# Optimization experiments

Measured on AMD Instinct MI355X. Metric: run time of the kernel, lower is better.

Reference implementation:

```python
import jax, jax.numpy as jnp
import numpy as np

B, N, C, K, S = 4, 4096, 256, 16, 1  # batch, points, channels, knn, share_planes
A = C // S  # attn_planes
EPS = 1e-5


def setup_inputs() -> dict:
    key = jax.random.key(0)
    ks = jax.random.split(key, 16)
    rn = lambda k, shape, s=0.05: (jax.random.normal(k, shape, jnp.float32) * s)
    return {
        "xyz": jax.random.uniform(ks[0], (B, N, 3), jnp.float32),
        "features": jax.random.normal(ks[1], (B, N, C), jnp.float32),
        "wq": rn(ks[2], (C, C)), "bq": jnp.zeros((C,), jnp.float32),
        "wk": rn(ks[3], (C, C)), "bk": jnp.zeros((C,), jnp.float32),
        "wv": rn(ks[4], (C, C)), "bv": jnp.zeros((C,), jnp.float32),
        "d1_w": rn(ks[5], (3, 3), 0.3), "d1_b": jnp.zeros((3,), jnp.float32),
        "bn_d_g": jnp.ones((3,), jnp.float32), "bn_d_b": jnp.zeros((3,), jnp.float32),
        "d2_w": rn(ks[6], (3, C), 0.3), "d2_b": jnp.zeros((C,), jnp.float32),
        "g_bn1_g": jnp.ones((C,), jnp.float32), "g_bn1_b": jnp.zeros((C,), jnp.float32),
        "g1_w": rn(ks[7], (C, A)), "g1_b": jnp.zeros((A,), jnp.float32),
        "g_bn2_g": jnp.ones((A,), jnp.float32), "g_bn2_b": jnp.zeros((A,), jnp.float32),
        "g2_w": rn(ks[8], (A, A)), "g2_b": jnp.zeros((A,), jnp.float32),
    }


def _bn(x, g, b):
    # BatchNorm2d_P in training mode: channels-last tensor (B,N,K,Ch),
    # normalize over all dims except the channel axis (biased variance).
    m = jnp.mean(x, axis=(0, 1, 2))
    v = jnp.var(x, axis=(0, 1, 2))
    return (x - m) * jax.lax.rsqrt(v + EPS) * g + b


def reference(xyz, features, wq, bq, wk, bk, wv, bv,
              d1_w, d1_b, bn_d_g, bn_d_b, d2_w, d2_b,
              g_bn1_g, g_bn1_b, g1_w, g1_b, g_bn2_g, g_bn2_b, g2_w, g2_b):
    # --- KNN (square_distance + topk smallest) ---
    sq = jnp.sum(xyz * xyz, axis=-1)                                  # (B,N)
    dist = sq[:, :, None] + sq[:, None, :] - 2.0 * jnp.einsum('bnd,bmd->bnm', xyz, xyz)
    idx = jax.lax.top_k(-dist, K)[1]                                  # (B,N,K)

    gather = jax.vmap(lambda pts, i: pts[i])                          # index_points
    knn_xyz = gather(xyz, idx)                                        # (B,N,K,3)

    q = features @ wq + bq                                            # (B,N,C)
    k = gather(features @ wk + bk, idx)                               # (B,N,K,C)
    v = gather(features @ wv + bv, idx)                               # (B,N,K,C)

    # fc_delta: Linear(3,3) -> BN -> ReLU -> Linear(3,C)
    rel = xyz[:, :, None, :] - knn_xyz                                # (B,N,K,3)
    pos_enc = jax.nn.relu(_bn(rel @ d1_w + d1_b, bn_d_g, bn_d_b)) @ d2_w + d2_b  # (B,N,K,C)

    # grouped sum of pos_enc over share_planes (identity when S=1)
    pe_sum = pos_enc.reshape(B, N, K, S, C // S).sum(axis=3)          # (B,N,K,C/S)

    # fc_gamma: BN -> ReLU -> Linear(C,A) -> BN -> ReLU -> Linear(A,A)
    h = q[:, :, None, :] - k + pe_sum                                 # (B,N,K,C)
    h = jax.nn.relu(_bn(h, g_bn1_g, g_bn1_b)) @ g1_w + g1_b           # (B,N,K,A)
    attn = jax.nn.relu(_bn(h, g_bn2_g, g_bn2_b)) @ g2_w + g2_b        # (B,N,K,A)
    attn = jax.nn.softmax(attn, axis=-2)                              # softmax over K

    vg = (v + pos_enc).reshape(B, N, K, S, C // S)                    # (B,N,K,S,C/S)
    out = jnp.einsum('bnksa,bnka->bnsa', vg, attn)                    # (B,N,S,C/S)
    return out.reshape(B, N, C)
```

## Files before the change

### kernel.cpp

```cpp
#include <hip/hip_runtime.h>
#include <hip/hip_bf16.h>
#include <math.h>

#define BB 4
#define NN 4096
#define CC 256
#define KK 16
#define AA 256
#define NPTS (BB*NN)
#define BNKTOT (NPTS*KK)
#define EPSF 1e-5f
#define MINVF (1.0f/262144.0f)

#define WPB 4
#define MROWS (WPB*KK)
#define IMG_PER_KSTEP (256*40)
#define IMG_TOTAL (8*IMG_PER_KSTEP)

#define ST_BND_SUM 0
#define ST_BND_SQ  8
#define ST_G1_SUM  16
#define ST_G1_SQ   272
#define ST_G2_SUM  528
#define ST_G2_SQ   784
#define CO_BND_S   0
#define CO_BND_B   4
#define CO_G1_S    16
#define CO_G1_B    272
#define CO_G2_S    528
#define CO_G2_B    784

typedef unsigned short u16;
typedef __attribute__((ext_vector_type(8))) short bf16x8;
typedef __attribute__((ext_vector_type(4))) float f32x4;

__device__ inline u16 f2bf(float x) {
    unsigned u = __float_as_uint(x);
    unsigned r = (u + 0x7FFFu + ((u >> 16) & 1u)) >> 16;
    return (u16)r;
}

__device__ inline float waveReduceAdd(float v) {
    #pragma unroll
    for (int o = 32; o > 0; o >>= 1) v += __shfl_down(v, o);
    return v;
}

__device__ inline bool lexlt(float d1, int i1, float d2, int i2) {
    return (d1 < d2) || (d1 == d2 && i1 < i2);
}

__global__ __launch_bounds__(256, 2) void qkv_mfma(
    const float* __restrict__ feat, const u16* __restrict__ wimg_all,
    const float* __restrict__ bq, const float* __restrict__ bk, const float* __restrict__ bv,
    float* __restrict__ oq, float* __restrict__ ok, float* __restrict__ ov)
{
    const int t = threadIdx.x;
    const int l = t & 63, w = t >> 6;
    const int p0 = blockIdx.x * 64;
    const u16* img = wimg_all + (size_t)blockIdx.y * IMG_TOTAL;
    const float* bias = blockIdx.y == 0 ? bq : (blockIdx.y == 1 ? bk : bv);
    float* out = blockIdx.y == 0 ? oq : (blockIdx.y == 1 ? ok : ov);

    __shared__ __align__(16) u16 A_lds[64 * 256];
    __shared__ __align__(16) u16 B_lds[IMG_PER_KSTEP];

    for (int r = 0; r < 64; ++r)
        A_lds[(r * 256 + t) ^ ((r & 7) << 3)] = f2bf(feat[(size_t)(p0 + r) * CC + t]);
    __syncthreads();

    f32x4 acc[4][4];
    #pragma unroll
    for (int q = 0; q < 4; ++q) {
        const float gb = bias[(w*4 + q) * 16 + (l & 15)];
        #pragma unroll
        for (int m = 0; m < 4; ++m) acc[m][q] = (f32x4){gb, gb, gb, gb};
    }

    for (int s = 0; s < 8; ++s) {
        #pragma unroll
        for (int i = 0; i < 5; ++i) {
            const int e = t + i * 256;
            *(uint4*)&B_lds[e * 8] = *(const uint4*)&img[(size_t)s * IMG_PER_KSTEP + e * 8];
        }
        __syncthreads();
        bf16x8 bf[4];
        #pragma unroll
        for (int q = 0; q < 4; ++q)
            bf[q] = *(const bf16x8*)&B_lds[((w*4 + q) * 16 + (l & 15)) * 40 + (l >> 4) * 8];
        #pragma unroll
        for (int m = 0; m < 4; ++m) {
            const int r = m * 16 + (l & 15);
            const bf16x8 af = *(const bf16x8*)&A_lds[((r * 256 + s * 32 + (l >> 4) * 8)) ^ ((r & 7) << 3)];
            #pragma unroll
            for (int q = 0; q < 4; ++q)
                acc[m][q] = __builtin_amdgcn_mfma_f32_16x16x32_bf16(af, bf[q], acc[m][q], 0, 0, 0);
        }
        __syncthreads();
    }

    #pragma unroll
    for (int q = 0; q < 4; ++q) {
        const int a = (w*4 + q) * 16 + (l & 15);
        #pragma unroll
        for (int m = 0; m < 4; ++m)
            #pragma unroll
            for (int j = 0; j < 4; ++j)
                out[(size_t)(p0 + m*16 + (l >> 4)*4 + j) * CC + a] = acc[m][q][j];
    }
}

__global__ __launch_bounds__(256, 2) void qkv_kernel(
    const float* __restrict__ feat,
    const float* __restrict__ wq, const float* __restrict__ bq,
    const float* __restrict__ wk, const float* __restrict__ bk,
    const float* __restrict__ wv, const float* __restrict__ bv,
    float* __restrict__ oq, float* __restrict__ ok, float* __restrict__ ov)
{
    const float* W; const float* bias; float* out;
    if (blockIdx.y == 0)      { W = wq; bias = bq; out = oq; }
    else if (blockIdx.y == 1) { W = wk; bias = bk; out = ok; }
    else                      { W = wv; bias = bv; out = ov; }

    const int p0 = blockIdx.x * 64;
    const int t  = threadIdx.x;
    __shared__ __align__(16) float fs[64][65];

    float acc[64];
    #pragma unroll
    for (int p = 0; p < 64; ++p) acc[p] = 0.f;

    for (int it = 0; it < 4; ++it) {
        const int tp = t >> 2;
        #pragma unroll
        for (int q = 0; q < 4; ++q) {
            const int ch = (t & 3) + q * 4;
            float4 v = *(const float4*)&feat[(size_t)(p0 + tp) * CC + it * 64 + ch * 4];
            fs[tp][ch*4+0] = v.x; fs[tp][ch*4+1] = v.y; fs[tp][ch*4+2] = v.z; fs[tp][ch*4+3] = v.w;
        }
        __syncthreads();
        #pragma unroll 4
        for (int i = 0; i < 64; ++i) {
            const float w = W[(size_t)(it * 64 + i) * CC + t];
            #pragma unroll
            for (int p = 0; p < 64; ++p) acc[p] = fmaf(fs[p][i], w, acc[p]);
        }
        __syncthreads();
    }
    const float bv_ = bias[t];
    #pragma unroll
    for (int p = 0; p < 64; ++p) out[(size_t)(p0 + p) * CC + t] = acc[p] + bv_;
}

#define KNN_BUFCAP 48
__global__ __launch_bounds__(256) void knn_kernel(
    const float* __restrict__ xyz, int* __restrict__ idxout)
{
    const int t = threadIdx.x;
    const int l = t & 63;
    const int w = t >> 6;
    const int g = blockIdx.x * 4 + w;
    const int b = g >> 12;
    const int n = g & 4095;
    const float* xb = xyz + (size_t)b * NN * 3;

    const float qx = xb[n*3+0], qy = xb[n*3+1], qz = xb[n*3+2];
    const float sqn = qx*qx + qy*qy + qz*qz;

    __shared__ float4 tile[512];
    __shared__ float bufd[4][KNN_BUFCAP];
    __shared__ int   bufi[4][KNN_BUFCAP];

    const float INF = 3.0e38f;
    float ld = INF; int li = 0x7fffffff;
    float kd = INF; int ki = 0x7fffffff;
    int cnt = 0;

    for (int t0 = 0; t0 < NN; t0 += 512) {
        #pragma unroll
        for (int r = 0; r < 2; ++r) {
            const int j = t + r * 256;
            const float x = xb[(t0 + j)*3 + 0];
            const float y = xb[(t0 + j)*3 + 1];
            const float z = xb[(t0 + j)*3 + 2];
            tile[j] = make_float4(x, y, z, x*x + y*y + z*z);
        }
        __syncthreads();
        for (int j0 = 0; j0 < 512; j0 += 64) {
            const float4 p = tile[j0 + l];
            const float d = sqn + p.w - 2.0f * (qx*p.x + qy*p.y + qz*p.z);
            const int  ci = t0 + j0 + l;
            bool pass = lexlt(d, ci, kd, ki);
            while (__any(pass)) {
                const unsigned long long m = __ballot(pass);
                const int rank  = (int)__popcll(m & ((1ull << l) - 1ull));
                const int total = (int)__popcll(m);
                const int space = KNN_BUFCAP - cnt;
                if (pass && rank < space) {
                    bufd[w][cnt + rank] = d;
                    bufi[w][cnt + rank] = ci;
                    pass = false;
                }
                cnt += total < space ? total : space;
                if (__any(pass)) {
                    float sd; int si;
                    if (l < 16)            { sd = ld; si = li; }
                    else if (l - 16 < cnt) { sd = bufd[w][l-16]; si = bufi[w][l-16]; }
                    else                   { sd = INF; si = 0x7fffffff; }
                    #pragma unroll
                    for (int k = 2; k <= 64; k <<= 1) {
                        #pragma unroll
                        for (int jj = k >> 1; jj > 0; jj >>= 1) {
                            const float od = __shfl_xor(sd, jj);
                            const int   oi = __shfl_xor(si, jj);
                            const bool keepMin = (((l & jj) == 0) == ((l & k) == 0));
                            const bool oSm = lexlt(od, oi, sd, si);
                            if (keepMin ? oSm : !oSm) { sd = od; si = oi; }
                        }
                    }
                    ld = (l < 16) ? sd : INF;
                    li = (l < 16) ? si : 0x7fffffff;
                    kd = __shfl(sd, 15);
                    ki = __shfl(si, 15);
                    cnt = 0;
                    pass = pass && lexlt(d, ci, kd, ki);
                }
            }
        }
        __syncthreads();
    }

    if (cnt > 0) {
        float sd; int si;
        if (l < 16)            { sd = ld; si = li; }
        else if (l - 16 < cnt) { sd = bufd[w][l-16]; si = bufi[w][l-16]; }
        else                   { sd = INF; si = 0x7fffffff; }
        #pragma unroll
        for (int k = 2; k <= 64; k <<= 1) {
            #pragma unroll
            for (int jj = k >> 1; jj > 0; jj >>= 1) {
                const float od = __shfl_xor(sd, jj);
                const int   oi = __shfl_xor(si, jj);
                const bool keepMin = (((l & jj) == 0) == ((l & k) == 0));
                const bool oSm = lexlt(od, oi, sd, si);
                if (keepMin ? oSm : !oSm) { sd = od; si = oi; }
            }
        }
        li = si;
    }
    if (l < 16) idxout[((size_t)b * NN + n) * KK + l] = li;
}

__global__ __launch_bounds__(256) void fc_delta_kernel(
    const float* __restrict__ xyz, const int* __restrict__ idx,
    const float* __restrict__ d1w, const float* __restrict__ d1b,
    float* __restrict__ t3, float* __restrict__ stats)
{
    const int t = threadIdx.x;
    float s[3] = {0.f, 0.f, 0.f}, sq[3] = {0.f, 0.f, 0.f};

    #pragma unroll
    for (int it = 0; it < 4; ++it) {
        const int g = blockIdx.x * 1024 + it * 256 + t;
        const int b = g >> 16;
        const int n = (g & 65535) >> 4;
        const int mi = idx[g];
        const float* xb = xyz + (size_t)b * NN * 3;
        const float rx = xb[n*3+0] - xb[mi*3+0];
        const float ry = xb[n*3+1] - xb[mi*3+1];
        const float rz = xb[n*3+2] - xb[mi*3+2];
        #pragma unroll
        for (int j = 0; j < 3; ++j) {
            const float tv = fmaf(rx, d1w[0*3+j], fmaf(ry, d1w[1*3+j], fmaf(rz, d1w[2*3+j], d1b[j])));
            t3[(size_t)g*3 + j] = tv;
            s[j] += tv;
            sq[j] = fmaf(tv, tv, sq[j]);
        }
    }

    __shared__ float red[4][6];
    const int lane = t & 63, wv = t >> 6;
    #pragma unroll
    for (int j = 0; j < 3; ++j) {
        const float rs  = waveReduceAdd(s[j]);
        const float rsq = waveReduceAdd(sq[j]);
        if (lane == 0) { red[wv][j] = rs; red[wv][3+j] = rsq; }
    }
    __syncthreads();
    if (t < 6) {
        const float v = red[0][t] + red[1][t] + red[2][t] + red[3][t];
        atomicAdd(&stats[t < 3 ? ST_BND_SUM + t : ST_BND_SQ + (t-3)], v);
    }
}

__global__ void finalize_bnd(const float* __restrict__ stats,
                             const float* __restrict__ g, const float* __restrict__ b,
                             float* __restrict__ consts)
{
    const int t = threadIdx.x;
    if (t < 3) {
        const float m = stats[ST_BND_SUM + t] * MINVF;
        const float v = stats[ST_BND_SQ + t] * MINVF - m * m;
        const float s = g[t] / sqrtf(v + EPSF);
        consts[CO_BND_S + t] = s;
        consts[CO_BND_B + t] = b[t] - m * s;
    }
}

__global__ __launch_bounds__(256, 2) void bn1_stats_kernel(
    const float* __restrict__ qproj, const float* __restrict__ kproj,
    const float* __restrict__ t3, const int* __restrict__ idx,
    const float* __restrict__ consts,
    const float* __restrict__ d2w, const float* __restrict__ d2b,
    float* __restrict__ stats)
{
    const int b   = blockIdx.x >> 8;
    const int pt0 = (blockIdx.x & 255) * 16;
    const int t = threadIdx.x;

    __shared__ float a3[768];
    __shared__ int idxs[256];

    const float bs[3]  = {consts[CO_BND_S+0], consts[CO_BND_S+1], consts[CO_BND_S+2]};
    const float bsh[3] = {consts[CO_BND_B+0], consts[CO_BND_B+1], consts[CO_BND_B+2]};
    const float* t3b = t3 + (size_t)(b * NN + pt0) * KK * 3;
    #pragma unroll
    for (int q = 0; q < 3; ++q) {
        const int f = t + q * 256;
        const int j = f % 3;
        a3[f] = fmaxf(fmaf(t3b[f], bs[j], bsh[j]), 0.f);
    }
    idxs[t] = idx[(size_t)(b * NN + pt0) * KK + t];
    __syncthreads();

    const int c = t;
    const float d20 = d2w[c], d21 = d2w[CC + c], d22 = d2w[2*CC + c], d2bc = d2b[c];
    float s = 0.f, sq = 0.f;
    for (int p = 0; p < 16; ++p) {
        const float qv = qproj[(size_t)(b * NN + pt0 + p) * CC + c];
        #pragma unroll
        for (int k = 0; k < 16; ++k) {
            const int mi = idxs[p*16 + k];
            const float kv = kproj[((size_t)b * NN + mi) * CC + c];
            const int f = (p*16 + k) * 3;
            const float pe = fmaf(a3[f], d20, fmaf(a3[f+1], d21, fmaf(a3[f+2], d22, d2bc)));
            const float h = qv - kv + pe;
            s += h; sq = fmaf(h, h, sq);
        }
    }
    atomicAdd(&stats[ST_G1_SUM + c], s);
    atomicAdd(&stats[ST_G1_SQ + c], sq);
}

__global__ void finalize_g(const float* __restrict__ ssum, const float* __restrict__ ssq,
                           const float* __restrict__ g, const float* __restrict__ b,
                           float* __restrict__ os, float* __restrict__ ob)
{
    const int c = threadIdx.x;
    const float m = ssum[c] * MINVF;
    const float v = ssq[c] * MINVF - m * m;
    const float s = g[c] / sqrtf(v + EPSF);
    os[c] = s;
    ob[c] = b[c] - m * s;
}

__global__ __launch_bounds__(256) void prep_weights(
    const float* __restrict__ wq, const float* __restrict__ wk,
    const float* __restrict__ wv, const float* __restrict__ g1w,
    const float* __restrict__ g2w, u16* __restrict__ img_all)
{
    const int s = blockIdx.x;
    const int mat = blockIdx.y;
    const float* W = mat == 0 ? wq : mat == 1 ? wk : mat == 2 ? wv : mat == 3 ? g1w : g2w;
    u16* img = img_all + (size_t)mat * IMG_TOTAL + (size_t)s * IMG_PER_KSTEP;
    const int n = threadIdx.x;
    #pragma unroll
    for (int i = 0; i < 32; ++i) {
        img[n*40 + i] = f2bf(W[(size_t)(s*32 + i) * AA + n]);
    }
}

__global__ __launch_bounds__(256, 2) void stage3_mfma(
    const float* __restrict__ qproj, const float* __restrict__ kproj,
    const float* __restrict__ t3, const int* __restrict__ idx,
    const float* __restrict__ consts, float* __restrict__ stats,
    const float* __restrict__ d2w, const float* __restrict__ d2b,
    const u16* __restrict__ g1img, const float* __restrict__ g1b,
    __hip_bfloat16* __restrict__ h2)
{
    const int t = threadIdx.x;
    const int l = t & 63, w = t >> 6;
    const int pt0 = blockIdx.x * WPB;
    const int bI = pt0 >> 12;

    __shared__ __align__(16) u16 A_lds[MROWS * 256];
    __shared__ __align__(16) u16 B_lds[IMG_PER_KSTEP];
    __shared__ int   idxs[MROWS];
    __shared__ float a3s[MROWS * 3];

    if (t < MROWS) idxs[t] = idx[(size_t)pt0 * KK + t];
    if (t < MROWS * 3) {
        const int j = t % 3;
        a3s[t] = fmaxf(fmaf(t3[(size_t)pt0 * 48 + t], consts[CO_BND_S + j], consts[CO_BND_B + j]), 0.f);
    }
    __syncthreads();

    {
        const float d20 = d2w[t], d21 = d2w[CC + t], d22 = d2w[2*CC + t], d2bc = d2b[t];
        const float g1s = consts[CO_G1_S + t], g1sh = consts[CO_G1_B + t];
        float qv[WPB];
        #pragma unroll
        for (int p = 0; p < WPB; ++p) qv[p] = qproj[(size_t)(pt0 + p) * CC + t];
        for (int r = 0; r < MROWS; ++r) {
            const int mi = idxs[r];
            const float kv = kproj[((size_t)bI * NN + mi) * CC + t];
            const float pe = fmaf(a3s[r*3], d20, fmaf(a3s[r*3+1], d21, fmaf(a3s[r*3+2], d22, d2bc)));
            const float h = qv[r >> 4] - kv + pe;
            const float av = fmaxf(fmaf(h, g1s, g1sh), 0.f);
            A_lds[(r * 256 + t) ^ ((r & 7) << 3)] = f2bf(av);
        }
    }
    __syncthreads();

    f32x4 acc[4][4];
    #pragma unroll
    for (int q = 0; q < 4; ++q) {
        const float gb = g1b[(w*4 + q) * 16 + (l & 15)];
        #pragma unroll
        for (int m = 0; m < 4; ++m) acc[m][q] = (f32x4){gb, gb, gb, gb};
    }

    for (int s = 0; s < 8; ++s) {
        #pragma unroll
        for (int i = 0; i < 5; ++i) {
            const int e = t + i * 256;
            *(uint4*)&B_lds[e * 8] = *(const uint4*)&g1img[(size_t)s * IMG_PER_KSTEP + e * 8];
        }
        __syncthreads();
        bf16x8 bf[4];
        #pragma unroll
        for (int q = 0; q < 4; ++q)
            bf[q] = *(const bf16x8*)&B_lds[((w*4 + q) * 16 + (l & 15)) * 40 + (l >> 4) * 8];
        #pragma unroll
        for (int m = 0; m < 4; ++m) {
            const int r = m * 16 + (l & 15);
            const bf16x8 af = *(const bf16x8*)&A_lds[((r * 256 + s * 32 + (l >> 4) * 8)) ^ ((r & 7) << 3)];
            #pragma unroll
            for (int q = 0; q < 4; ++q)
                acc[m][q] = __builtin_amdgcn_mfma_f32_16x16x32_bf16(af, bf[q], acc[m][q], 0, 0, 0);
        }
        __syncthreads();
    }

    #pragma unroll
    for (int q = 0; q < 4; ++q) {
        const int a = (w*4 + q) * 16 + (l & 15);
        float sc = 0.f, sq = 0.f;
        #pragma unroll
        for (int m = 0; m < 4; ++m) {
            #pragma unroll
            for (int j = 0; j < 4; ++j) {
                const float v = acc[m][q][j];
                sc += v; sq = fmaf(v, v, sq);
                h2[((size_t)(pt0 + m) * KK + ((l >> 4) * 4 + j)) * AA + a] = __float2bfloat16(v);
            }
        }
        sc += __shfl_xor(sc, 16); sc += __shfl_xor(sc, 32);
        sq += __shfl_xor(sq, 16); sq += __shfl_xor(sq, 32);
        if (l < 16) {
            atomicAdd(&stats[ST_G2_SUM + a], sc);
            atomicAdd(&stats[ST_G2_SQ + a], sq);
        }
    }
}

__global__ __launch_bounds__(256, 2) void stage4_mfma(
    const float* __restrict__ vproj,
    const float* __restrict__ t3, const int* __restrict__ idx,
    const float* __restrict__ consts,
    const float* __restrict__ d2w, const float* __restrict__ d2b,
    const u16* __restrict__ g2img, const float* __restrict__ g2b,
    const __hip_bfloat16* __restrict__ h2, float* __restrict__ out)
{
    const int t = threadIdx.x;
    const int l = t & 63, w = t >> 6;
    const int pt0 = blockIdx.x * WPB;
    const int bI = pt0 >> 12;

    __shared__ __align__(16) u16 A_lds[MROWS * 256];
    __shared__ __align__(16) u16 B_lds[IMG_PER_KSTEP];
    __shared__ int   idxs[MROWS];
    __shared__ float a3s[MROWS * 3];

    if (t < MROWS) idxs[t] = idx[(size_t)pt0 * KK + t];
    if (t < MROWS * 3) {
        const int j = t % 3;
        a3s[t] = fmaxf(fmaf(t3[(size_t)pt0 * 48 + t], consts[CO_BND_S + j], consts[CO_BND_B + j]), 0.f);
    }
    __syncthreads();

    {
        const float g2s = consts[CO_G2_S + t], g2sh = consts[CO_G2_B + t];
        for (int r = 0; r < MROWS; ++r) {
            const float hv = __bfloat162float(h2[((size_t)pt0 * KK + r) * AA + t]);
            const float av = fmaxf(fmaf(hv, g2s, g2sh), 0.f);
            A_lds[(r * 256 + t) ^ ((r & 7) << 3)] = f2bf(av);
        }
    }
    __syncthreads();

    f32x4 acc[4][4];
    #pragma unroll
    for (int q = 0; q < 4; ++q) {
        const float gb = g2b[(w*4 + q) * 16 + (l & 15)];
        #pragma unroll
        for (int m = 0; m < 4; ++m) acc[m][q] = (f32x4){gb, gb, gb, gb};
    }

    for (int s = 0; s < 8; ++s) {
        #pragma unroll
        for (int i = 0; i < 5; ++i) {
            const int e = t + i * 256;
            *(uint4*)&B_lds[e * 8] = *(const uint4*)&g2img[(size_t)s * IMG_PER_KSTEP + e * 8];
        }
        __syncthreads();
        bf16x8 bf[4];
        #pragma unroll
        for (int q = 0; q < 4; ++q)
            bf[q] = *(const bf16x8*)&B_lds[((w*4 + q) * 16 + (l & 15)) * 40 + (l >> 4) * 8];
        #pragma unroll
        for (int m = 0; m < 4; ++m) {
            const int r = m * 16 + (l & 15);
            const bf16x8 af = *(const bf16x8*)&A_lds[((r * 256 + s * 32 + (l >> 4) * 8)) ^ ((r & 7) << 3)];
            #pragma unroll
            for (int q = 0; q < 4; ++q)
                acc[m][q] = __builtin_amdgcn_mfma_f32_16x16x32_bf16(af, bf[q], acc[m][q], 0, 0, 0);
        }
        __syncthreads();
    }

    #pragma unroll
    for (int q = 0; q < 4; ++q) {
        const int a = (w*4 + q) * 16 + (l & 15);
        const float dw0 = d2w[a], dw1 = d2w[CC + a], dw2 = d2w[2*CC + a], db = d2b[a];
        #pragma unroll
        for (int m = 0; m < 4; ++m) {
            f32x4 lg = acc[m][q];
            float mx = fmaxf(fmaxf(lg[0], lg[1]), fmaxf(lg[2], lg[3]));
            mx = fmaxf(mx, __shfl_xor(mx, 16));
            mx = fmaxf(mx, __shfl_xor(mx, 32));
            float e[4]; float ss = 0.f;
            #pragma unroll
            for (int j = 0; j < 4; ++j) { e[j] = expf(lg[j] - mx); ss += e[j]; }
            ss += __shfl_xor(ss, 16); ss += __shfl_xor(ss, 32);
            const float inv = 1.0f / ss;
            float part = 0.f;
            #pragma unroll
            for (int j = 0; j < 4; ++j) {
                const int kk = (l >> 4) * 4 + j;
                const int mi = idxs[m * 16 + kk];
                const float vv = vproj[((size_t)bI * NN + mi) * CC + a];
                const float pe = fmaf(a3s[(m*16+kk)*3], dw0,
                                 fmaf(a3s[(m*16+kk)*3+1], dw1,
                                 fmaf(a3s[(m*16+kk)*3+2], dw2, db)));
                part = fmaf(e[j] * inv, vv + pe, part);
            }
            part += __shfl_xor(part, 16); part += __shfl_xor(part, 32);
            if (l < 16) out[(size_t)(pt0 + m) * CC + a] = part;
        }
    }
}

__global__ __launch_bounds__(256, 2) void stage3_fp32(
    const float* __restrict__ qproj, const float* __restrict__ kproj,
    const float* __restrict__ t3, const int* __restrict__ idx,
    const float* __restrict__ consts, float* __restrict__ stats,
    const float* __restrict__ d2w, const float* __restrict__ d2b,
    const float* __restrict__ g1w, const float* __restrict__ g1b)
{
    const size_t pt = blockIdx.x;
    const int b = (int)(pt >> 12);
    const int t = threadIdx.x;
    __shared__ float a3[48];
    __shared__ int idxs[16];
    __shared__ __align__(16) float hr[16][256];
    if (t < 48) {
        const int j = t % 3;
        a3[t] = fmaxf(fmaf(t3[pt*48 + t], consts[CO_BND_S + j], consts[CO_BND_B + j]), 0.f);
    }
    if (t < 16) idxs[t] = idx[pt*16 + t];
    __syncthreads();
    {
        const float d20 = d2w[t], d21 = d2w[CC + t], d22 = d2w[2*CC + t], d2bc = d2b[t];
        const float g1s = consts[CO_G1_S + t], g1sh = consts[CO_G1_B + t];
        const float qv = qproj[pt * CC + t];
        #pragma unroll
        for (int k = 0; k < 16; ++k) {
            const int mi = idxs[k];
            const float kv = kproj[((size_t)b * NN + mi) * CC + t];
            const float pe = fmaf(a3[k*3], d20, fmaf(a3[k*3+1], d21, fmaf(a3[k*3+2], d22, d2bc)));
            hr[k][t] = fmaxf(fmaf(qv - kv + pe, g1s, g1sh), 0.f);
        }
    }
    __syncthreads();
    float acc[16];
    const float gb = g1b[t];
    #pragma unroll
    for (int k = 0; k < 16; ++k) acc[k] = gb;
    #pragma unroll 4
    for (int c4 = 0; c4 < 64; ++c4) {
        const float* wp = g1w + (size_t)(c4*4) * AA + t;
        const float w0 = wp[0], w1 = wp[AA], w2 = wp[2*AA], w3 = wp[3*AA];
        #pragma unroll
        for (int k = 0; k < 16; ++k) {
            const float4 hv = *(const float4*)&hr[k][c4*4];
            acc[k] = fmaf(hv.x, w0, fmaf(hv.y, w1, fmaf(hv.z, w2, fmaf(hv.w, w3, acc[k]))));
        }
    }
    float s = 0.f, sq = 0.f;
    #pragma unroll
    for (int k = 0; k < 16; ++k) { s += acc[k]; sq = fmaf(acc[k], acc[k], sq); }
    atomicAdd(&stats[ST_G2_SUM + t], s);
    atomicAdd(&stats[ST_G2_SQ + t], sq);
}

__global__ __launch_bounds__(256, 2) void stage4_fp32(
    const float* __restrict__ qproj, const float* __restrict__ kproj,
    const float* __restrict__ vproj,
    const float* __restrict__ t3, const int* __restrict__ idx,
    const float* __restrict__ consts,
    const float* __restrict__ d2w, const float* __restrict__ d2b,
    const float* __restrict__ g1w, const float* __restrict__ g1b,
    const float* __restrict__ g2w, const float* __restrict__ g2b,
    float* __restrict__ out)
{
    const size_t pt = blockIdx.x;
    const int b = (int)(pt >> 12);
    const int t = threadIdx.x;
    __shared__ float a3[48];
    __shared__ int idxs[16];
    __shared__ __align__(16) float r2[16][256];
    if (t < 48) {
        const int j = t % 3;
        a3[t] = fmaxf(fmaf(t3[pt*48 + t], consts[CO_BND_S + j], consts[CO_BND_B + j]), 0.f);
    }
    if (t < 16) idxs[t] = idx[pt*16 + t];
    __syncthreads();
    const float g2s = consts[CO_G2_S + t], g2sh = consts[CO_G2_B + t];
    {
        __shared__ __align__(16) float hr[16][256];
        {
            const float d20 = d2w[t], d21 = d2w[CC + t], d22 = d2w[2*CC + t], d2bc = d2b[t];
            const float g1s = consts[CO_G1_S + t], g1sh = consts[CO_G1_B + t];
            const float qv = qproj[pt * CC + t];
            #pragma unroll
            for (int k = 0; k < 16; ++k) {
                const int mi = idxs[k];
                const float kv = kproj[((size_t)b * NN + mi) * CC + t];
                const float pe = fmaf(a3[k*3], d20, fmaf(a3[k*3+1], d21, fmaf(a3[k*3+2], d22, d2bc)));
                hr[k][t] = fmaxf(fmaf(qv - kv + pe, g1s, g1sh), 0.f);
            }
        }
        __syncthreads();
        float acc[16];
        const float gb = g1b[t];
        #pragma unroll
        for (int k = 0; k < 16; ++k) acc[k] = gb;
        #pragma unroll 4
        for (int c4 = 0; c4 < 64; ++c4) {
            const float* wp = g1w + (size_t)(c4*4) * AA + t;
            const float w0 = wp[0], w1 = wp[AA], w2 = wp[2*AA], w3 = wp[3*AA];
            #pragma unroll
            for (int k = 0; k < 16; ++k) {
                const float4 hv = *(const float4*)&hr[k][c4*4];
                acc[k] = fmaf(hv.x, w0, fmaf(hv.y, w1, fmaf(hv.z, w2, fmaf(hv.w, w3, acc[k]))));
            }
        }
        __syncthreads();
        #pragma unroll
        for (int k = 0; k < 16; ++k) r2[k][t] = fmaxf(fmaf(acc[k], g2s, g2sh), 0.f);
        __syncthreads();
    }
    float lg[16];
    const float gb2 = g2b[t];
    #pragma unroll
    for (int k = 0; k < 16; ++k) lg[k] = gb2;
    #pragma unroll 4
    for (int c4 = 0; c4 < 64; ++c4) {
        const float* wp = g2w + (size_t)(c4*4) * AA + t;
        const float w0 = wp[0], w1 = wp[AA], w2 = wp[2*AA], w3 = wp[3*AA];
        #pragma unroll
        for (int k = 0; k < 16; ++k) {
            const float4 hv = *(const float4*)&r2[k][c4*4];
            lg[k] = fmaf(hv.x, w0, fmaf(hv.y, w1, fmaf(hv.z, w2, fmaf(hv.w, w3, lg[k]))));
        }
    }
    float mx = lg[0];
    #pragma unroll
    for (int k = 1; k < 16; ++k) mx = fmaxf(mx, lg[k]);
    float sum = 0.f;
    #pragma unroll
    for (int k = 0; k < 16; ++k) { lg[k] = expf(lg[k] - mx); sum += lg[k]; }
    const float inv = 1.0f / sum;
    const float d20 = d2w[t], d21 = d2w[CC + t], d22 = d2w[2*CC + t], d2bc = d2b[t];
    float o = 0.f;
    #pragma unroll
    for (int k = 0; k < 16; ++k) {
        const int mi = idxs[k];
        const float vv = vproj[((size_t)b * NN + mi) * CC + t];
        const float pe = fmaf(a3[k*3], d20, fmaf(a3[k*3+1], d21, fmaf(a3[k*3+2], d22, d2bc)));
        o = fmaf(vv + pe, lg[k] * inv, o);
    }
    out[pt * CC + t] = o;
}

extern "C" void kernel_launch(void* const* d_in, const int* in_sizes, int n_in,
                              void* d_out, int out_size, void* d_ws, size_t ws_size,
                              hipStream_t stream)
{
    const float* xyz   = (const float*)d_in[0];
    const float* feat  = (const float*)d_in[1];
    const float* wq    = (const float*)d_in[2];
    const float* bq    = (const float*)d_in[3];
    const float* wk    = (const float*)d_in[4];
    const float* bk    = (const float*)d_in[5];
    const float* wv    = (const float*)d_in[6];
    const float* bv    = (const float*)d_in[7];
    const float* d1w   = (const float*)d_in[8];
    const float* d1b   = (const float*)d_in[9];
    const float* bndg  = (const float*)d_in[10];
    const float* bndb  = (const float*)d_in[11];
    const float* d2w   = (const float*)d_in[12];
    const float* d2b   = (const float*)d_in[13];
    const float* g1g   = (const float*)d_in[14];
    const float* g1bb  = (const float*)d_in[15];
    const float* g1w   = (const float*)d_in[16];
    const float* g1b   = (const float*)d_in[17];
    const float* g2g   = (const float*)d_in[18];
    const float* g2bb  = (const float*)d_in[19];
    const float* g2w   = (const float*)d_in[20];
    const float* g2b   = (const float*)d_in[21];
    float* out = (float*)d_out;

    float* qproj = (float*)d_ws;
    float* kproj = qproj + (size_t)NPTS * CC;
    float* vproj = kproj + (size_t)NPTS * CC;
    float* t3    = vproj + (size_t)NPTS * CC;
    float* stats = t3 + (size_t)BNKTOT * 3;
    float* consts = stats + 2048;
    int*   idxb  = (int*)(consts + 2048);
    u16*   wimg  = (u16*)(idxb + BNKTOT);
    u16*   g1img = wimg + (size_t)3 * IMG_TOTAL;
    u16*   g2img = wimg + (size_t)4 * IMG_TOTAL;
    __hip_bfloat16* h2 = (__hip_bfloat16*)(wimg + (size_t)5 * IMG_TOTAL);
    const size_t need_store = (size_t)((char*)h2 - (char*)d_ws) + (size_t)BNKTOT * AA * 2;
    const bool store = ws_size >= need_store;

    hipMemsetAsync(stats, 0, 2048 * sizeof(float), stream);

    if (store) {
        prep_weights<<<dim3(8, 5), 256, 0, stream>>>(wq, wk, wv, g1w, g2w, wimg);
        qkv_mfma<<<dim3(NPTS / 64, 3), 256, 0, stream>>>(feat, wimg, bq, bk, bv,
                                                         qproj, kproj, vproj);
    } else {
        dim3 gq(NPTS / 64, 3);
        qkv_kernel<<<gq, 256, 0, stream>>>(feat, wq, bq, wk, bk, wv, bv, qproj, kproj, vproj);
    }

    knn_kernel<<<NPTS / 4, 256, 0, stream>>>(xyz, idxb);

    fc_delta_kernel<<<BNKTOT / 1024, 256, 0, stream>>>(xyz, idxb, d1w, d1b, t3, stats);

    finalize_bnd<<<1, 64, 0, stream>>>(stats, bndg, bndb, consts);

    bn1_stats_kernel<<<1024, 256, 0, stream>>>(qproj, kproj, t3, idxb, consts, d2w, d2b, stats);

    finalize_g<<<1, 256, 0, stream>>>(stats + ST_G1_SUM, stats + ST_G1_SQ, g1g, g1bb,
                                      consts + CO_G1_S, consts + CO_G1_B);

    if (store)
        stage3_mfma<<<NPTS / WPB, 256, 0, stream>>>(qproj, kproj, t3, idxb, consts, stats,
                                                    d2w, d2b, g1img, g1b, h2);
    else
        stage3_fp32<<<NPTS, 256, 0, stream>>>(qproj, kproj, t3, idxb, consts, stats,
                                              d2w, d2b, g1w, g1b);

    finalize_g<<<1, 256, 0, stream>>>(stats + ST_G2_SUM, stats + ST_G2_SQ, g2g, g2bb,
                                      consts + CO_G2_S, consts + CO_G2_B);

    if (store)
        stage4_mfma<<<NPTS / WPB, 256, 0, stream>>>(vproj, t3, idxb, consts,
                                                    d2w, d2b, g2img, g2b, h2, out);
    else
        stage4_fp32<<<NPTS, 256, 0, stream>>>(qproj, kproj, vproj, t3, idxb, consts,
                                              d2w, d2b, g1w, g1b, g2w, g2b, out);
}
```

Baseline: 681.9 us.

## Load MFMA weight fragments directly from global memory instead of LDS staging

The three MFMA GEMM kernels now read their bf16x8 B fragments straight from a repacked global weight image instead of copying each k-step slice into shared memory. prep_weights emits the image in fragment order, and the padded 40-element stride goes away. This removes two barriers per k-step and roughly 20 KB of LDS per block, which may raise occupancy. In exchange, each wave issues its own global/L2 loads for weights, and different waves no longer share a single copy.

```diff
diff --git a/kernel.cpp b/kernel.cpp
--- a/kernel.cpp
+++ b/kernel.cpp
@@ -14,7 +14,7 @@
 
 #define WPB 4
 #define MROWS (WPB*KK)
-#define IMG_PER_KSTEP (256*40)
+#define IMG_PER_KSTEP (256*32)
 #define IMG_TOTAL (8*IMG_PER_KSTEP)
 
 #define ST_BND_SUM 0
@@ -63,7 +63,6 @@
     float* out = blockIdx.y == 0 ? oq : (blockIdx.y == 1 ? ok : ov);
 
     __shared__ __align__(16) u16 A_lds[64 * 256];
-    __shared__ __align__(16) u16 B_lds[IMG_PER_KSTEP];
 
     for (int r = 0; r < 64; ++r)
         A_lds[(r * 256 + t) ^ ((r & 7) << 3)] = f2bf(feat[(size_t)(p0 + r) * CC + t]);
@@ -78,16 +77,12 @@
     }
 
     for (int s = 0; s < 8; ++s) {
-        #pragma unroll
-        for (int i = 0; i < 5; ++i) {
-            const int e = t + i * 256;
-            *(uint4*)&B_lds[e * 8] = *(const uint4*)&img[(size_t)s * IMG_PER_KSTEP + e * 8];
-        }
-        __syncthreads();
         bf16x8 bf[4];
         #pragma unroll
-        for (int q = 0; q < 4; ++q)
-            bf[q] = *(const bf16x8*)&B_lds[((w*4 + q) * 16 + (l & 15)) * 40 + (l >> 4) * 8];
+        for (int q = 0; q < 4; ++q) {
+            const int nq = (w*4 + q) * 16 + (l & 15);
+            bf[q] = *(const bf16x8*)&img[(size_t)s * IMG_PER_KSTEP + ((nq*4 + (l >> 4)) * 8)];
+        }
         #pragma unroll
         for (int m = 0; m < 4; ++m) {
             const int r = m * 16 + (l & 15);
@@ -96,7 +91,6 @@
             for (int q = 0; q < 4; ++q)
                 acc[m][q] = __builtin_amdgcn_mfma_f32_16x16x32_bf16(af, bf[q], acc[m][q], 0, 0, 0);
         }
-        __syncthreads();
     }
 
     #pragma unroll
@@ -375,9 +369,10 @@
     u16* img = img_all + (size_t)mat * IMG_TOTAL + (size_t)s * IMG_PER_KSTEP;
     const int n = threadIdx.x;
     #pragma unroll
-    for (int i = 0; i < 32; ++i) {
-        img[n*40 + i] = f2bf(W[(size_t)(s*32 + i) * AA + n]);
-    }
+    for (int h = 0; h < 4; ++h)
+        #pragma unroll
+        for (int j = 0; j < 8; ++j)
+            img[(n*4 + h)*8 + j] = f2bf(W[(size_t)(s*32 + h*8 + j) * AA + n]);
 }
 
 __global__ __launch_bounds__(256, 2) void stage3_mfma(
@@ -394,7 +389,6 @@
     const int bI = pt0 >> 12;
 
     __shared__ __align__(16) u16 A_lds[MROWS * 256];
-    __shared__ __align__(16) u16 B_lds[IMG_PER_KSTEP];
     __shared__ int   idxs[MROWS];
     __shared__ float a3s[MROWS * 3];
 
@@ -431,16 +425,12 @@
     }
 
     for (int s = 0; s < 8; ++s) {
-        #pragma unroll
-        for (int i = 0; i < 5; ++i) {
-            const int e = t + i * 256;
-            *(uint4*)&B_lds[e * 8] = *(const uint4*)&g1img[(size_t)s * IMG_PER_KSTEP + e * 8];
-        }
-        __syncthreads();
         bf16x8 bf[4];
         #pragma unroll
-        for (int q = 0; q < 4; ++q)
-            bf[q] = *(const bf16x8*)&B_lds[((w*4 + q) * 16 + (l & 15)) * 40 + (l >> 4) * 8];
+        for (int q = 0; q < 4; ++q) {
+            const int nq = (w*4 + q) * 16 + (l & 15);
+            bf[q] = *(const bf16x8*)&g1img[(size_t)s * IMG_PER_KSTEP + ((nq*4 + (l >> 4)) * 8)];
+        }
         #pragma unroll
         for (int m = 0; m < 4; ++m) {
             const int r = m * 16 + (l & 15);
@@ -449,7 +439,6 @@
             for (int q = 0; q < 4; ++q)
                 acc[m][q] = __builtin_amdgcn_mfma_f32_16x16x32_bf16(af, bf[q], acc[m][q], 0, 0, 0);
         }
-        __syncthreads();
     }
 
     #pragma unroll
@@ -488,7 +477,6 @@
     const int bI = pt0 >> 12;
 
     __shared__ __align__(16) u16 A_lds[MROWS * 256];
-    __shared__ __align__(16) u16 B_lds[IMG_PER_KSTEP];
     __shared__ int   idxs[MROWS];
     __shared__ float a3s[MROWS * 3];
 
@@ -518,16 +506,12 @@
     }
 
     for (int s = 0; s < 8; ++s) {
-        #pragma unroll
-        for (int i = 0; i < 5; ++i) {
-            const int e = t + i * 256;
-            *(uint4*)&B_lds[e * 8] = *(const uint4*)&g2img[(size_t)s * IMG_PER_KSTEP + e * 8];
-        }
-        __syncthreads();
         bf16x8 bf[4];
         #pragma unroll
-        for (int q = 0; q < 4; ++q)
-            bf[q] = *(const bf16x8*)&B_lds[((w*4 + q) * 16 + (l & 15)) * 40 + (l >> 4) * 8];
+        for (int q = 0; q < 4; ++q) {
+            const int nq = (w*4 + q) * 16 + (l & 15);
+            bf[q] = *(const bf16x8*)&g2img[(size_t)s * IMG_PER_KSTEP + ((nq*4 + (l >> 4)) * 8)];
+        }
         #pragma unroll
         for (int m = 0; m < 4; ++m) {
             const int r = m * 16 + (l & 15);
@@ -536,7 +520,6 @@
             for (int q = 0; q < 4; ++q)
                 acc[m][q] = __builtin_amdgcn_mfma_f32_16x16x32_bf16(af, bf[q], acc[m][q], 0, 0, 0);
         }
-        __syncthreads();
     }
 
     #pragma unroll
```

Result: faster. 593.6 us (-12.9%).
